# Kernel tuning notes

Hardware: AMD Instinct MI355X
Metric: run time of the kernel (lower is better)

## Reference

```python
import jax, jax.numpy as jnp
import numpy as np

WS = 4        # window_size
SS = 2        # shift_size
NH = 8        # num_heads
EPS = 1e-5    # LayerNorm eps (torch default)


def _rel_pos_index(ws):
    coords = np.stack(np.meshgrid(np.arange(ws), np.arange(ws), indexing='ij')).reshape(2, -1)
    rel = (coords[:, :, None] - coords[:, None, :]).transpose(1, 2, 0)
    rel[..., 0] += ws - 1
    rel[..., 1] += ws - 1
    rel[..., 0] *= 2 * ws - 1
    return rel.sum(-1)  # [N, N] ints

REL_IDX = _rel_pos_index(WS)


def _shift_mask(Hp, Wp, ws, ss):
    # standard Swin shifted-window region mask: 0 within region, -100 across regions
    img = np.zeros((Hp, Wp))
    cnt = 0
    for hs in (slice(0, -ws), slice(-ws, -ss), slice(-ss, None)):
        for wsl in (slice(0, -ws), slice(-ws, -ss), slice(-ss, None)):
            img[hs, wsl] = cnt
            cnt += 1
    mw = img.reshape(Hp // ws, ws, Wp // ws, ws).transpose(0, 2, 1, 3).reshape(-1, ws * ws)
    d = mw[:, None, :] - mw[:, :, None]
    return np.where(d != 0, -100.0, 0.0).astype(np.float32)  # [nW, N, N]


def _ln(x, g, b):
    m = jnp.mean(x, -1, keepdims=True)
    v = jnp.mean((x - m) ** 2, -1, keepdims=True)
    return (x - m) * jax.lax.rsqrt(v + EPS) * g + b


def setup_inputs() -> dict:
    key = jax.random.key(0)
    ks = jax.random.split(key, 8)
    D, F = 512, 1024
    rn = lambda k, s: (jax.random.normal(k, s, jnp.float32) * 0.02)
    return {
        'x': jax.random.normal(ks[0], (4, 64 * 128, D), jnp.float32),
        'g1': jnp.ones((D,), jnp.float32), 'beta1': jnp.zeros((D,), jnp.float32),
        'w_qkv': rn(ks[1], (3 * D, D)), 'b_qkv': jnp.zeros((3 * D,), jnp.float32),
        'rpb': rn(ks[2], ((2 * WS - 1) ** 2, NH)),
        'w_proj': rn(ks[3], (D, D)), 'b_proj': jnp.zeros((D,), jnp.float32),
        'g2': jnp.ones((D,), jnp.float32), 'beta2': jnp.zeros((D,), jnp.float32),
        'w1': rn(ks[4], (F, D)), 'b1': jnp.zeros((F,), jnp.float32),
        'w2': rn(ks[5], (D, F)), 'b2': jnp.zeros((D,), jnp.float32),
        'H': 64, 'W': 128,
    }


def reference(x, g1, beta1, w_qkv, b_qkv, rpb, w_proj, b_proj, g2, beta2, w1, b1, w2, b2, H, W):
    B, L, C = x.shape
    hd = C // NH
    scale = hd ** (-0.5)
    N = WS * WS
    Hp, Wp = H, W  # H, W chosen divisible by WS -> no padding branch
    nW = (Hp // WS) * (Wp // WS)

    shortcut = x
    h = _ln(x, g1, beta1).reshape(B, H, W, C)
    # cyclic shift
    h = jnp.roll(h, (-SS, -SS), axis=(1, 2))
    # window partition -> [B*nW, N, C]
    xw = h.reshape(B, Hp // WS, WS, Wp // WS, WS, C).transpose(0, 1, 3, 2, 4, 5).reshape(-1, N, C)

    qkv = (xw @ w_qkv.T + b_qkv).reshape(-1, N, 3, NH, hd).transpose(2, 0, 3, 1, 4)
    q, k, v = qkv[0] * scale, qkv[1], qkv[2]          # [B*nW, NH, N, hd]
    attn = jnp.einsum('whnd,whmd->whnm', q, k)        # [B*nW, NH, N, N]

    bias = rpb[REL_IDX.reshape(-1)].reshape(N, N, NH).transpose(2, 0, 1)  # [NH, N, N]
    attn = attn + bias[None]

    mask = jnp.asarray(_shift_mask(Hp, Wp, WS, SS))   # [nW, N, N]
    attn = attn.reshape(B, nW, NH, N, N) + mask[None, :, None]
    attn = jax.nn.softmax(attn.reshape(-1, NH, N, N), axis=-1)

    o = jnp.einsum('whnm,whmd->whnd', attn, v).transpose(0, 2, 1, 3).reshape(-1, N, C)
    o = o @ w_proj.T + b_proj
    # window reverse + reverse shift
    o = o.reshape(B, Hp // WS, Wp // WS, WS, WS, C).transpose(0, 1, 3, 2, 4, 5).reshape(B, Hp, Wp, C)
    o = jnp.roll(o, (SS, SS), axis=(1, 2)).reshape(B, H * W, C)

    x = shortcut + o
    h2 = _ln(x, g2, beta2)
    m = jax.nn.gelu(h2 @ w1.T + b1, approximate=False) @ w2.T + b2
    return x + m
```

## Files before the change

### kernel.cpp

```cpp
#include <hip/hip_runtime.h>
#include <hip/hip_bf16.h>
#include <math.h>

typedef __bf16 bf16_t;
typedef __bf16 bf16x8 __attribute__((ext_vector_type(8)));
typedef float f32x4 __attribute__((ext_vector_type(4)));


#define X1_OFF   0u
#define XW_OFF   67108864u
#define QKV_OFF  100663296u
#define WQ_OFF   201326592u
#define WP_OFF   202899456u
#define W1_OFF   203423744u
#define W2_OFF   204472320u
#define SV_OFF   205520896u
#define FLAG_OFF 205545472u

__device__ __forceinline__ int perm_row(int r) {
    int b   = r >> 13;
    int rem = r & 8191;
    int w   = rem >> 4;
    int n   = rem & 15;
    int wy  = w >> 5, wx = w & 31;
    int y   = wy * 4 + (n >> 2);
    int x   = wx * 4 + (n & 3);
    int ys  = (y + 2) & 63;
    int xs  = (x + 2) & 127;
    return (b << 13) + (ys << 7) + xs;
}

__device__ __forceinline__ void gld16(const void* g, void* l) {
    __builtin_amdgcn_global_load_lds(
        (const __attribute__((address_space(1))) unsigned int*)(unsigned long long)(uintptr_t)g,
        (__attribute__((address_space(3))) unsigned int*)(unsigned int)(uintptr_t)l,
        16, 0, 0);
}

#define SBAR __builtin_amdgcn_sched_barrier(0)
#define BARRIER do { SBAR; __builtin_amdgcn_s_barrier(); SBAR; } while (0)

__global__ __launch_bounds__(256) void k_probe(const unsigned short* __restrict__ x,
                                               int n, int* __restrict__ flag) {
    __shared__ int cnt;
    if (threadIdx.x == 0) cnt = 0;
    __syncthreads();
    int c = 0;
    for (int i = threadIdx.x; i < n; i += 256) {
        int e = (x[i] >> 7) & 0xFF;
        if (e >= 0xC0) c++;
    }
    atomicAdd(&cnt, c);
    __syncthreads();
    if (threadIdx.x == 0) *flag = (cnt > 8) ? 1 : 0;
}

__global__ __launch_bounds__(256) void k_cvt_bf16(const void* __restrict__ src,
                                                  bf16_t* __restrict__ dst, int n,
                                                  const int* __restrict__ flag) {
    int i = blockIdx.x * 256 + threadIdx.x;
    if (i >= n) return;
    dst[i] = (*flag) ? (bf16_t)((const float*)src)[i] : ((const bf16_t*)src)[i];
}

__global__ __launch_bounds__(256) void k_cvt_small(
        const void* g1, const void* be1, const void* bq, const void* bp,
        const void* g2, const void* be2, const void* b1, const void* b2,
        const void* rpb, float* __restrict__ dst, const int* __restrict__ flag) {
    int i = blockIdx.x * 256 + threadIdx.x;
    const void* src; int off;
    if      (i < 512)  { src = g1;  off = i; }
    else if (i < 1024) { src = be1; off = i - 512; }
    else if (i < 2560) { src = bq;  off = i - 1024; }
    else if (i < 3072) { src = bp;  off = i - 2560; }
    else if (i < 3584) { src = g2;  off = i - 3072; }
    else if (i < 4096) { src = be2; off = i - 3584; }
    else if (i < 5120) { src = b1;  off = i - 4096; }
    else if (i < 5632) { src = b2;  off = i - 5120; }
    else if (i < 6024) { src = rpb; off = i - 5632; }
    else return;
    dst[i] = (*flag) ? ((const float*)src)[off] : (float)((const bf16_t*)src)[off];
}

__global__ __launch_bounds__(256) void k_ln1(const void* __restrict__ x,
                                             const float* __restrict__ g,
                                             const float* __restrict__ be,
                                             bf16_t* __restrict__ xw,
                                             const int* __restrict__ flag) {
    int r    = blockIdx.x * 4 + (threadIdx.x >> 6);
    int lane = threadIdx.x & 63;
    int f    = *flag;
    long ro  = (long)perm_row(r) * 512;
    const float*  x32 = (const float*)x + ro;
    const bf16_t* x16 = (const bf16_t*)x + ro;
    int base = lane * 8;
    float v[8];
    float s = 0.f, ss = 0.f;
#pragma unroll
    for (int j = 0; j < 8; j++) {
        float t = f ? x32[base + j] : (float)x16[base + j];
        v[j] = t; s += t; ss += t * t;
    }
#pragma unroll
    for (int off = 32; off; off >>= 1) {
        s  += __shfl_down(s,  off, 64);
        ss += __shfl_down(ss, off, 64);
    }
    s  = __shfl(s, 0, 64);
    ss = __shfl(ss, 0, 64);
    float m   = s * (1.f / 512.f);
    float var = ss * (1.f / 512.f) - m * m;
    float inv = rsqrtf(var + 1e-5f);
    bf16_t* orow = xw + (long)r * 512;
#pragma unroll
    for (int j = 0; j < 8; j++)
        orow[base + j] = (bf16_t)((v[j] - m) * inv * g[base + j] + be[base + j]);
}

__global__ __launch_bounds__(256) void k_ln2(const float* __restrict__ x1,
                                             const float* __restrict__ g,
                                             const float* __restrict__ be,
                                             bf16_t* __restrict__ h2) {
    int r    = blockIdx.x * 4 + (threadIdx.x >> 6);
    int lane = threadIdx.x & 63;
    const float* xr = x1 + (long)r * 512;
    int base = lane * 8;
    float v[8];
    float s = 0.f, ss = 0.f;
#pragma unroll
    for (int j = 0; j < 8; j++) {
        float t = xr[base + j];
        v[j] = t; s += t; ss += t * t;
    }
#pragma unroll
    for (int off = 32; off; off >>= 1) {
        s  += __shfl_down(s,  off, 64);
        ss += __shfl_down(ss, off, 64);
    }
    s  = __shfl(s, 0, 64);
    ss = __shfl(ss, 0, 64);
    float m   = s * (1.f / 512.f);
    float var = ss * (1.f / 512.f) - m * m;
    float inv = rsqrtf(var + 1e-5f);
    bf16_t* orow = h2 + (long)r * 512;
#pragma unroll
    for (int j = 0; j < 8; j++)
        orow[base + j] = (bf16_t)((v[j] - m) * inv * g[base + j] + be[base + j]);
}

template<int EPI>
__global__ __launch_bounds__(512, 2) void k_gemm256(const bf16_t* __restrict__ A,
                                                    const bf16_t* __restrict__ Wt,
                                                    const float* __restrict__ bias,
                                                    void* __restrict__ out,
                                                    const void* __restrict__ res,
                                                    const int* __restrict__ flag,
                                                    int N, int K) {
    __shared__ __attribute__((aligned(16))) char smem[131072];
    int tid  = threadIdx.x;
    int lane = tid & 63, wv = tid >> 6;

    int nbx = N >> 8;
    int id  = blockIdx.x;
    int xb  = (id >> 3) % nbx;
    int yb  = ((id >> 3) / nbx) * 8 + (id & 7);
    int m0  = yb << 8, n0 = xb << 8;

    int srow = tid >> 3;
    int cg   = (tid & 7) ^ (srow & 7);
    const bf16_t* gA = A  + (long)(m0 + srow) * K + cg * 8;
    const bf16_t* gB = Wt + (long)(n0 + srow) * K + cg * 8;
    long r64 = (long)64 * K;

    int rr = lane & 15, quad = lane >> 4;
    int wh = wv >> 2, wq = wv & 3;
    int lA  = (wh * 64 + rr) * 128;
    int lB  = (wq * 32 + rr) * 128;
    int ck0 = (quad ^ (rr & 7)) * 16;
    int ck1 = ck0 ^ 64;

    f32x4 acc[8][4];
#pragma unroll
    for (int mi = 0; mi < 8; mi++)
#pragma unroll
        for (int ni = 0; ni < 4; ni++) { f32x4 z = {0.f,0.f,0.f,0.f}; acc[mi][ni] = z; }

    int S = K >> 6;

    gld16(gA,             smem + 0     + wv * 1024);
    gld16(gA + r64,       smem + 8192  + wv * 1024);
    gld16(gB,             smem + 32768 + wv * 1024);
    gld16(gB + r64,       smem + 40960 + wv * 1024);
    gld16(gB + 2 * r64,   smem + 49152 + wv * 1024);
    gld16(gB + 3 * r64,   smem + 57344 + wv * 1024);
    gld16(gA + 2 * r64,   smem + 16384 + wv * 1024);
    gld16(gA + 3 * r64,   smem + 24576 + wv * 1024);
    asm volatile("s_waitcnt vmcnt(4)" ::: "memory");
    BARRIER;

    bf16x8 af[4][2], bg[2][2];

#define FRAG_A(AH)                                                            \
    _Pragma("unroll") for (int mi = 0; mi < 4; mi++) {                        \
        af[mi][0] = *(const bf16x8*)(bc + (AH)*16384 + lA + mi*2048 + ck0);   \
        af[mi][1] = *(const bf16x8*)(bc + (AH)*16384 + lA + mi*2048 + ck1);   \
    }
#define FRAG_B(BH)                                                            \
    _Pragma("unroll") for (int ni = 0; ni < 2; ni++) {                        \
        bg[ni][0] = *(const bf16x8*)(bc + 32768 + (BH)*16384 + lB + ni*2048 + ck0); \
        bg[ni][1] = *(const bf16x8*)(bc + 32768 + (BH)*16384 + lB + ni*2048 + ck1); \
    }
#define MFMA_CL(AH, BH)                                                       \
    do {                                                                      \
        asm volatile("s_waitcnt lgkmcnt(0)" ::: "memory"); SBAR;              \
        __builtin_amdgcn_s_setprio(1);                                        \
        _Pragma("unroll") for (int mi = 0; mi < 4; mi++)                      \
            _Pragma("unroll") for (int ni = 0; ni < 2; ni++)                  \
                _Pragma("unroll") for (int kk = 0; kk < 2; kk++)              \
                    acc[(AH)*4 + mi][(BH)*2 + ni] =                           \
                        __builtin_amdgcn_mfma_f32_16x16x32_bf16(              \
                            af[mi][kk], bg[ni][kk], acc[(AH)*4 + mi][(BH)*2 + ni], 0, 0, 0); \
        __builtin_amdgcn_s_setprio(0);                                        \
    } while (0)
#define STAGE(GP, SLOT)                                                       \
    do { gld16((GP) + kn,       bn + (SLOT) + wv * 1024);                     \
         gld16((GP) + r64 + kn, bn + (SLOT) + 8192 + wv * 1024); } while (0)

    for (int t = 0; t < S; ++t) {
        char* bc = smem + (t & 1) * 65536;
        char* bn = smem + ((t & 1) ^ 1) * 65536;
        long  kn = (long)(t + 1) * 64;
        bool  st = (t + 1 < S);
        FRAG_A(0); FRAG_B(0);
        if (st) { STAGE(gA, 0);
                  asm volatile("s_waitcnt vmcnt(4)" ::: "memory"); }
        else    { asm volatile("s_waitcnt vmcnt(2)" ::: "memory"); }
        BARRIER;
        MFMA_CL(0, 0);
        FRAG_B(1);
        if (st) { STAGE(gB, 32768);
                  asm volatile("s_waitcnt vmcnt(4)" ::: "memory"); }
        else    { asm volatile("s_waitcnt vmcnt(0)" ::: "memory"); }
        BARRIER;
        MFMA_CL(0, 1);
        FRAG_A(1); FRAG_B(0);
        if (st) STAGE(gB + 2 * r64, 49152);
        BARRIER;
        MFMA_CL(1, 0);
        FRAG_B(1);
        if (st) { STAGE(gA + 2 * r64, 16384);
                  asm volatile("s_waitcnt vmcnt(4)" ::: "memory"); }
        BARRIER;
        MFMA_CL(1, 1);
    }
    BARRIER;
#undef FRAG_A
#undef FRAG_B
#undef MFMA_CL
#undef STAGE

    float* sc = (float*)(smem + wv * 16384);
    int f    = (EPI == 1 || EPI == 3) ? *flag : 0;
    int j8   = lane & 7;
    int rl   = lane >> 3;
    int colg = n0 + wq * 32 + (j8 >> 2) * 128 + ((j8 * 8) & 31);
    f32x4 b0 = *(const f32x4*)(bias + colg);
    f32x4 b1 = *(const f32x4*)(bias + colg + 4);

#pragma unroll
    for (int ah = 0; ah < 2; ++ah) {
#pragma unroll
        for (int bh = 0; bh < 2; ++bh)
#pragma unroll
            for (int ni = 0; ni < 2; ++ni)
#pragma unroll
                for (int mi = 0; mi < 4; ++mi)
#pragma unroll
                    for (int i = 0; i < 4; ++i) {
                        int r  = mi * 16 + quad * 4 + i;
                        int cl = bh * 32 + ni * 16 + rr;
                        sc[r * 64 + ((((cl >> 2) ^ (r & 15)) << 2) | (cl & 3))] =
                            acc[ah * 4 + mi][bh * 2 + ni][i];
                    }
#pragma unroll
        for (int p = 0; p < 8; ++p) {
            int r = p * 8 + rl;
            f32x4 v0 = *(const f32x4*)(sc + r * 64 + (((2 * j8)     ^ (r & 15)) << 2));
            f32x4 v1 = *(const f32x4*)(sc + r * 64 + (((2 * j8 + 1) ^ (r & 15)) << 2));
            int row = m0 + ah * 128 + wh * 64 + r;
            v0 += b0; v1 += b1;

            if (EPI == 0) {
                bf16x8 ob;
#pragma unroll
                for (int c = 0; c < 4; c++) { ob[c] = (bf16_t)v0[c]; ob[c + 4] = (bf16_t)v1[c]; }
                *(bf16x8*)((bf16_t*)out + (long)row * N + colg) = ob;
            } else if (EPI == 1) {
                long o = (long)perm_row(row) * 512 + colg;
                if (f) {
                    f32x4 r0 = *(const f32x4*)((const float*)res + o);
                    f32x4 r1 = *(const f32x4*)((const float*)res + o + 4);
                    v0 += r0; v1 += r1;
                } else {
                    bf16x8 rb = *(const bf16x8*)((const bf16_t*)res + o);
#pragma unroll
                    for (int c = 0; c < 4; c++) { v0[c] += (float)rb[c]; v1[c] += (float)rb[c + 4]; }
                }
                *(f32x4*)((float*)out + o)     = v0;
                *(f32x4*)((float*)out + o + 4) = v1;
            } else if (EPI == 2) {
                bf16x8 ob;
#pragma unroll
                for (int c = 0; c < 4; c++) {
                    float a0 = v0[c], a1 = v1[c];
                    ob[c]     = (bf16_t)(0.5f * a0 * (1.f + erff(a0 * 0.70710678118654752f)));
                    ob[c + 4] = (bf16_t)(0.5f * a1 * (1.f + erff(a1 * 0.70710678118654752f)));
                }
                *(bf16x8*)((bf16_t*)out + (long)row * N + colg) = ob;
            } else {
                long o = (long)row * 512 + colg;
                f32x4 r0 = *(const f32x4*)((const float*)res + o);
                f32x4 r1 = *(const f32x4*)((const float*)res + o + 4);
                v0 += r0; v1 += r1;
                if (f) {
                    *(f32x4*)((float*)out + o)     = v0;
                    *(f32x4*)((float*)out + o + 4) = v1;
                } else {
                    bf16x8 ob;
#pragma unroll
                    for (int c = 0; c < 4; c++) { ob[c] = (bf16_t)v0[c]; ob[c + 4] = (bf16_t)v1[c]; }
                    *(bf16x8*)((bf16_t*)out + o) = ob;
                }
            }
        }
    }
}

__global__ __launch_bounds__(256) void k_attn(const bf16_t* __restrict__ qkv,
                                              const float* __restrict__ rpb,
                                              bf16_t* __restrict__ O) {
    __shared__ float q[16][68], k[16][68], v[16][68];
    __shared__ float S[16][17];

    int blk = blockIdx.x;
    int h   = blk & 7;
    int w   = blk >> 3;
    int tid = threadIdx.x;

    int n0 = tid >> 4;
    int d0 = (tid & 15) * 4;
    const bf16_t* base = qkv + (long)(w * 16 + n0) * 1536 + h * 64 + d0;
#pragma unroll
    for (int j = 0; j < 4; j++) {
        q[n0][d0 + j] = (float)base[j] * 0.125f;
        k[n0][d0 + j] = (float)base[512 + j];
        v[n0][d0 + j] = (float)base[1024 + j];
    }
    __syncthreads();

    int i = tid >> 4, j = tid & 15;
    float s = 0.f;
#pragma unroll
    for (int d = 0; d < 64; d++) s += q[i][d] * k[j][d];

    int iy = i >> 2, ix = i & 3, jy = j >> 2, jx = j & 3;
    s += rpb[((iy - jy + 3) * 7 + (ix - jx + 3)) * 8 + h];

    int wl = w & 511;
    int wy = wl >> 5, wx = wl & 31;
    int yi = wy * 4 + iy, xi = wx * 4 + ix;
    int yj = wy * 4 + jy, xj = wx * 4 + jx;
    int ri = (yi < 60 ? 0 : (yi < 62 ? 1 : 2)) * 3 + (xi < 124 ? 0 : (xi < 126 ? 1 : 2));
    int rj = (yj < 60 ? 0 : (yj < 62 ? 1 : 2)) * 3 + (xj < 124 ? 0 : (xj < 126 ? 1 : 2));
    if (ri != rj) s -= 100.f;
    S[i][j] = s;
    __syncthreads();

    if (tid < 16) {
        float mx = -1e30f;
#pragma unroll
        for (int c = 0; c < 16; c++) mx = fmaxf(mx, S[tid][c]);
        float sum = 0.f;
#pragma unroll
        for (int c = 0; c < 16; c++) { float e = expf(S[tid][c] - mx); S[tid][c] = e; sum += e; }
        float invs = 1.f / sum;
#pragma unroll
        for (int c = 0; c < 16; c++) S[tid][c] *= invs;
    }
    __syncthreads();

#pragma unroll
    for (int t = 0; t < 4; t++) {
        int e  = tid + t * 256;
        int oi = e >> 6, od = e & 63;
        float acc = 0.f;
#pragma unroll
        for (int c = 0; c < 16; c++) acc += S[oi][c] * v[c][od];
        O[(long)(w * 16 + oi) * 512 + h * 64 + od] = (bf16_t)acc;
    }
}

extern "C" void kernel_launch(void* const* d_in, const int* in_sizes, int n_in,
                              void* d_out, int out_size, void* d_ws, size_t ws_size,
                              hipStream_t stream) {
    char* ws = (char*)d_ws;
    float*  x1   = (float*)(ws + X1_OFF);
    bf16_t* xw   = (bf16_t*)(ws + XW_OFF);
    bf16_t* qkv  = (bf16_t*)(ws + QKV_OFF);
    bf16_t* wq_b = (bf16_t*)(ws + WQ_OFF);
    bf16_t* wp_b = (bf16_t*)(ws + WP_OFF);
    bf16_t* w1_b = (bf16_t*)(ws + W1_OFF);
    bf16_t* w2_b = (bf16_t*)(ws + W2_OFF);
    float*  sv   = (float*)(ws + SV_OFF);
    int*    flag = (int*)(ws + FLAG_OFF);

    k_probe<<<1, 256, 0, stream>>>((const unsigned short*)d_in[0], 4096, flag);
    k_cvt_bf16<<<3072, 256, 0, stream>>>(d_in[3],  wq_b, 786432, flag);
    k_cvt_bf16<<<1024, 256, 0, stream>>>(d_in[6],  wp_b, 262144, flag);
    k_cvt_bf16<<<2048, 256, 0, stream>>>(d_in[10], w1_b, 524288, flag);
    k_cvt_bf16<<<2048, 256, 0, stream>>>(d_in[12], w2_b, 524288, flag);
    k_cvt_small<<<24,  256, 0, stream>>>(d_in[1], d_in[2], d_in[4], d_in[7],
                                         d_in[8], d_in[9], d_in[11], d_in[13],
                                         d_in[5], sv, flag);

    k_ln1<<<dim3(8192), dim3(256), 0, stream>>>(d_in[0], sv, sv + 512, xw, flag);
    k_gemm256<0><<<dim3(768), dim3(512), 0, stream>>>(xw, wq_b, sv + 1024, qkv, nullptr, flag, 1536, 512);
    k_attn<<<dim3(16384), dim3(256), 0, stream>>>(qkv, sv + 5632, xw );
    k_gemm256<1><<<dim3(256), dim3(512), 0, stream>>>(xw, wp_b, sv + 2560, x1, d_in[0], flag, 512, 512);
    k_ln2<<<dim3(8192), dim3(256), 0, stream>>>(x1, sv + 3072, sv + 3584, xw );
    k_gemm256<2><<<dim3(512), dim3(512), 0, stream>>>(xw, w1_b, sv + 4096, qkv , nullptr, flag, 1024, 512);
    k_gemm256<3><<<dim3(256), dim3(512), 0, stream>>>(qkv, w2_b, sv + 5120, d_out, x1, flag, 512, 1024);
}
```

Before: 453.3 us.

## Vectorize loads/stores, use tanh GELU, reorder GEMM MFMA clusters

Vectorizes the LayerNorm and attention loads and stores into 8- and 4-wide bf16/f32 accesses, and hoists the dtype flag branch out of the per-element loops. Replaces the exact erf GELU in the FC1 epilogue with a tanh approximation built on exp2. Reorders the fragment loads and MFMA clusters in the GEMM main loop so one B fragment is reused across consecutive clusters. The tanh GELU differs numerically from the exact erf form the reference specifies.

```diff
diff --git a/kernel.cpp b/kernel.cpp
--- a/kernel.cpp
+++ b/kernel.cpp
@@ -4,6 +4,7 @@
 
 typedef __bf16 bf16_t;
 typedef __bf16 bf16x8 __attribute__((ext_vector_type(8)));
+typedef __bf16 bf16x4 __attribute__((ext_vector_type(4)));
 typedef float f32x4 __attribute__((ext_vector_type(4)));
 
 
@@ -40,6 +41,14 @@
 #define SBAR __builtin_amdgcn_sched_barrier(0)
 #define BARRIER do { SBAR; __builtin_amdgcn_s_barrier(); SBAR; } while (0)
 
+__device__ __forceinline__ float fast_gelu(float x) {
+    float y = 0.7978845608f * (x + 0.044715f * x * x * x);
+    y = fminf(fmaxf(y, -15.f), 15.f);
+    float u = __builtin_amdgcn_exp2f(y * 2.885390082f);
+    float t = (u - 1.f) / (u + 1.f);
+    return 0.5f * x * (1.f + t);
+}
+
 __global__ __launch_bounds__(256) void k_probe(const unsigned short* __restrict__ x,
                                                int n, int* __restrict__ flag) {
     __shared__ int cnt;
@@ -60,7 +69,8 @@
                                                   const int* __restrict__ flag) {
     int i = blockIdx.x * 256 + threadIdx.x;
     if (i >= n) return;
-    dst[i] = (*flag) ? (bf16_t)((const float*)src)[i] : ((const bf16_t*)src)[i];
+    if (*flag) dst[i] = (bf16_t)((const float*)src)[i];
+    else       dst[i] = ((const bf16_t*)src)[i];
 }
 
 __global__ __launch_bounds__(256) void k_cvt_small(
@@ -79,7 +89,8 @@
     else if (i < 5632) { src = b2;  off = i - 5120; }
     else if (i < 6024) { src = rpb; off = i - 5632; }
     else return;
-    dst[i] = (*flag) ? ((const float*)src)[off] : (float)((const bf16_t*)src)[off];
+    if (*flag) dst[i] = ((const float*)src)[off];
+    else       dst[i] = (float)((const bf16_t*)src)[off];
 }
 
 __global__ __launch_bounds__(256) void k_ln1(const void* __restrict__ x,
@@ -89,18 +100,21 @@
                                              const int* __restrict__ flag) {
     int r    = blockIdx.x * 4 + (threadIdx.x >> 6);
     int lane = threadIdx.x & 63;
-    int f    = *flag;
     long ro  = (long)perm_row(r) * 512;
-    const float*  x32 = (const float*)x + ro;
-    const bf16_t* x16 = (const bf16_t*)x + ro;
     int base = lane * 8;
     float v[8];
+    if (*flag) {
+        const float* p = (const float*)x + ro + base;
+#pragma unroll
+        for (int j = 0; j < 8; j++) v[j] = p[j];
+    } else {
+        bf16x8 p = *(const bf16x8*)((const bf16_t*)x + ro + base);
+#pragma unroll
+        for (int j = 0; j < 8; j++) v[j] = (float)p[j];
+    }
     float s = 0.f, ss = 0.f;
 #pragma unroll
-    for (int j = 0; j < 8; j++) {
-        float t = f ? x32[base + j] : (float)x16[base + j];
-        v[j] = t; s += t; ss += t * t;
-    }
+    for (int j = 0; j < 8; j++) { s += v[j]; ss += v[j] * v[j]; }
 #pragma unroll
     for (int off = 32; off; off >>= 1) {
         s  += __shfl_down(s,  off, 64);
@@ -112,9 +126,11 @@
     float var = ss * (1.f / 512.f) - m * m;
     float inv = rsqrtf(var + 1e-5f);
     bf16_t* orow = xw + (long)r * 512;
+    bf16x8 o;
 #pragma unroll
     for (int j = 0; j < 8; j++)
-        orow[base + j] = (bf16_t)((v[j] - m) * inv * g[base + j] + be[base + j]);
+        o[j] = (bf16_t)((v[j] - m) * inv * g[base + j] + be[base + j]);
+    *(bf16x8*)(orow + base) = o;
 }
 
 __global__ __launch_bounds__(256) void k_ln2(const float* __restrict__ x1,
@@ -143,9 +159,11 @@
     float var = ss * (1.f / 512.f) - m * m;
     float inv = rsqrtf(var + 1e-5f);
     bf16_t* orow = h2 + (long)r * 512;
+    bf16x8 o;
 #pragma unroll
     for (int j = 0; j < 8; j++)
-        orow[base + j] = (bf16_t)((v[j] - m) * inv * g[base + j] + be[base + j]);
+        o[j] = (bf16_t)((v[j] - m) * inv * g[base + j] + be[base + j]);
+    *(bf16x8*)(orow + base) = o;
 }
 
 template<int EPI>
@@ -243,15 +261,15 @@
         else    { asm volatile("s_waitcnt vmcnt(0)" ::: "memory"); }
         BARRIER;
         MFMA_CL(0, 1);
-        FRAG_A(1); FRAG_B(0);
+        FRAG_A(1);
         if (st) STAGE(gB + 2 * r64, 49152);
         BARRIER;
-        MFMA_CL(1, 0);
-        FRAG_B(1);
+        MFMA_CL(1, 1);
+        FRAG_B(0);
         if (st) { STAGE(gA + 2 * r64, 16384);
                   asm volatile("s_waitcnt vmcnt(4)" ::: "memory"); }
         BARRIER;
-        MFMA_CL(1, 1);
+        MFMA_CL(1, 0);
     }
     BARRIER;
 #undef FRAG_A
@@ -312,9 +330,8 @@
                 bf16x8 ob;
 #pragma unroll
                 for (int c = 0; c < 4; c++) {
-                    float a0 = v0[c], a1 = v1[c];
-                    ob[c]     = (bf16_t)(0.5f * a0 * (1.f + erff(a0 * 0.70710678118654752f)));
-                    ob[c + 4] = (bf16_t)(0.5f * a1 * (1.f + erff(a1 * 0.70710678118654752f)));
+                    ob[c]     = (bf16_t)fast_gelu(v0[c]);
+                    ob[c + 4] = (bf16_t)fast_gelu(v1[c]);
                 }
                 *(bf16x8*)((bf16_t*)out + (long)row * N + colg) = ob;
             } else {
@@ -350,12 +367,19 @@
     int n0 = tid >> 4;
     int d0 = (tid & 15) * 4;
     const bf16_t* base = qkv + (long)(w * 16 + n0) * 1536 + h * 64 + d0;
+    bf16x4 qv = *(const bf16x4*)(base);
+    bf16x4 kv = *(const bf16x4*)(base + 512);
+    bf16x4 vv = *(const bf16x4*)(base + 1024);
+    f32x4 qf, kf, vf;
 #pragma unroll
     for (int j = 0; j < 4; j++) {
-        q[n0][d0 + j] = (float)base[j] * 0.125f;
-        k[n0][d0 + j] = (float)base[512 + j];
-        v[n0][d0 + j] = (float)base[1024 + j];
-    }
+        qf[j] = (float)qv[j] * 0.125f;
+        kf[j] = (float)kv[j];
+        vf[j] = (float)vv[j];
+    }
+    *(f32x4*)&q[n0][d0] = qf;
+    *(f32x4*)&k[n0][d0] = kf;
+    *(f32x4*)&v[n0][d0] = vf;
     __syncthreads();
 
     int i = tid >> 4, j = tid & 15;
```

Result: faster. 427.8 us (-5.6%).
